# Kernel tuning notes

Hardware: AMD Instinct MI355X
Metric: run time of the kernel (lower is better)

## Reference

```python
import jax, jax.numpy as jnp
import numpy as np

B, F, H, E, C, K = 32768, 1024, 512, 10, 10, 4  # batch, in_features, hidden, f_enc, num_classes, n_branches


def setup_inputs() -> dict:
    key = jax.random.key(0)
    ks = jax.random.split(key, 12)
    def rn(k, shape, scale):
        return jax.random.normal(k, shape, jnp.float32) * scale
    return {
        "w0": rn(ks[0], (B, F), 1.0),
        "w1": rn(ks[1], (B, F), 1.0),
        "w2": rn(ks[2], (B, F), 1.0),
        "w3": rn(ks[3], (B, F), 1.0),
        # 4 branch linears in -> hidden, stacked on leading axis
        "Wlin": rn(ks[4], (K, H, F), F ** -0.5),
        "blin": jnp.zeros((K, H), jnp.float32),
        # per-branch Q/K/V projections hidden -> f_enc
        "Wq": rn(ks[5], (K, E, H), H ** -0.5),
        "bq": jnp.zeros((K, E), jnp.float32),
        "Wk": rn(ks[6], (K, E, H), H ** -0.5),
        "bk": jnp.zeros((K, E), jnp.float32),
        "Wv": rn(ks[7], (K, E, H), H ** -0.5),
        "bv": jnp.zeros((K, E), jnp.float32),
        # 4 final classifier heads f_enc -> num_classes
        "Wfin": rn(ks[8], (K, C, E), E ** -0.5),
        "bfin": jnp.zeros((K, C), jnp.float32),
    }


def reference(w0, w1, w2, w3, Wlin, blin, Wq, bq, Wk, bk, Wv, bv, Wfin, bfin):
    # dropout is identity in eval mode
    w = jnp.stack([w0, w1, w2, w3], axis=1)              # [B,K,F]
    h = jnp.einsum('bkf,khf->bkh', w, Wlin) + blin        # [B,K,H]
    q = jnp.einsum('bkh,keh->bke', h, Wq) + bq            # [B,K,E]
    k_enc = jnp.einsum('bkh,keh->bke', h, Wk) + bk        # [B,K,E]
    v = jnp.einsum('bkh,keh->bke', h, Wv) + bv            # [B,K,E]
    # einsum 'bij,bil->bjl' contracts the branch axis (i == K)
    attn = jnp.einsum('bke,bkl->bel', q, k_enc) / np.float32(np.sqrt(E))  # [B,E,E]
    attn = jax.nn.softmax(attn, axis=1)                   # torch Softmax(dim=1)
    att_out = jnp.einsum('bnm,bkm->bkn', attn, v)         # [B,K,E]
    w0o = att_out[:, 0, :]                                # original uses index 0 for all four heads
    logits = jnp.einsum('be,kce->bkc', w0o, Wfin) + bfin  # [B,K,C]
    outputs = jnp.mean(jax.nn.softmax(logits, axis=-1), axis=1)  # 0.25 * sum of 4 softmaxed heads
    return (outputs, attn)
```

## Files before the change

kernel.cpp:

```cpp
#include <hip/hip_runtime.h>
#include <stdint.h>

#define B_ROWS 32768
#define F_DIM  1024
#define H_DIM  512

typedef __attribute__((ext_vector_type(4))) float    floatx4;
typedef __attribute__((ext_vector_type(2))) __fp16   fp16x2;
typedef __attribute__((ext_vector_type(8))) _Float16 halfx8;

__device__ __forceinline__ void async_load16(const void* g, void* l) {
    __builtin_amdgcn_global_load_lds(
        (const __attribute__((address_space(1))) void*)g,
        (__attribute__((address_space(3))) void*)l, 16, 0, 0);
}

__device__ __forceinline__ floatx4 nt_load4(const float* p) {
    return __builtin_nontemporal_load((const floatx4*)p);
}

__global__ __launch_bounds__(128) void k_prep(
    const float* __restrict__ Wlin, const float* __restrict__ blin,
    const float* __restrict__ Wq, const float* __restrict__ Wk,
    const float* __restrict__ Wv, const float* __restrict__ bq,
    const float* __restrict__ bk, const float* __restrict__ bv,
    ushort* __restrict__ Wcomb16, float* __restrict__ bcomb)
{
    __shared__ float sw_[H_DIM];
    __shared__ float sbl[H_DIM];
    const int bx   = blockIdx.x;
    const int k    = bx >> 6;
    const int d    = (bx >> 1) & 31;
    const int half = bx & 1;
    const int t    = threadIdx.x;
    const int col  = half * 512 + t * 4;
    ushort4* outp = (ushort4*)(Wcomb16 + (((size_t)(k * 32 + d)) << 10) + col);

    if (d >= 30) {
        ushort4 z; z.x = z.y = z.z = z.w = 0;
        *outp = z;
        if (half == 0 && t == 0) bcomb[k * 32 + d] = 0.f;
        return;
    }

    const float* wrow; float bias;
    if (d < 10)      { wrow = Wq + (size_t)(k * 10 + d) * H_DIM;      bias = bq[k * 10 + d]; }
    else if (d < 20) { wrow = Wk + (size_t)(k * 10 + d - 10) * H_DIM; bias = bk[k * 10 + d - 10]; }
    else             { wrow = Wv + (size_t)(k * 10 + d - 20) * H_DIM; bias = bv[k * 10 + d - 20]; }

    const float* bl = blin + (size_t)k * H_DIM;
    for (int i = t; i < H_DIM; i += 128) { sw_[i] = wrow[i]; sbl[i] = bl[i]; }
    __syncthreads();

    const float* wl = Wlin + (((size_t)k * H_DIM) << 10) + col;

    floatx4 acc0 = {0.f,0.f,0.f,0.f}, acc1 = {0.f,0.f,0.f,0.f};
    float ba0 = 0.f, ba1 = 0.f;
    #pragma unroll 8
    for (int h = 0; h < H_DIM; h += 2) {
        const float s0 = sw_[h], s1 = sw_[h + 1];
        const floatx4 x0 = *(const floatx4*)(wl + ((size_t)h << 10));
        const floatx4 x1 = *(const floatx4*)(wl + ((size_t)(h + 1) << 10));
        acc0 += x0 * s0;
        acc1 += x1 * s1;
        ba0 += s0 * sbl[h];
        ba1 += s1 * sbl[h + 1];
    }
    const floatx4 acc = acc0 + acc1;
    union { _Float16 h[4]; ushort4 u; } o;
    o.h[0] = (_Float16)acc.x; o.h[1] = (_Float16)acc.y;
    o.h[2] = (_Float16)acc.z; o.h[3] = (_Float16)acc.w;
    *outp = o.u;
    if (half == 0 && t == 0) bcomb[k * 32 + d] = bias + ba0 + ba1;
}

#define SM_BS    0
#define SM_QKV   (64 * 1024)
#define SM_BC    (SM_QKV + 128 * 121 * 4)
#define SM_W     (SM_BC + 512)
#define SM_B     (SM_W + 1600)
#define SM_TOTAL (SM_B + 160)

__global__ __launch_bounds__(512) void k_all(
    const float* __restrict__ w0, const float* __restrict__ w1,
    const float* __restrict__ w2, const float* __restrict__ w3,
    const ushort* __restrict__ Wcomb16, const float* __restrict__ bcomb,
    const float* __restrict__ Wfin, const float* __restrict__ bfin,
    float* __restrict__ outputs, float* __restrict__ attn)
{
    __shared__ __align__(16) unsigned char smem[SM_TOTAL];
    ushort* Bs  = (ushort*)(smem + SM_BS);
    float*  QKV = (float*) (smem + SM_QKV);
    float*  sbc = (float*) (smem + SM_BC);
    float*  sW  = (float*) (smem + SM_W);
    float*  sb  = (float*) (smem + SM_B);
    float*  sA  = (float*) (smem + SM_BS);

    const int tid     = threadIdx.x;
    const int rowBase = blockIdx.x * 128;

    if (tid < 128) sbc[tid] = bcomb[tid];
    if (tid < 400) sW[tid]  = Wfin[tid];
    if (tid < 40)  sb[tid]  = bfin[tid];

    const int wv = tid >> 6;
    const int ln = tid & 63;
    const int lr = ln & 15;
    const int lq = ln >> 4;
    const int sw = lr & 7;

    #pragma unroll 1
    for (int k = 0; k < 4; ++k) {
        const float* A = (k == 0) ? w0 : (k == 1) ? w1 : (k == 2) ? w2 : w3;

        __syncthreads();
        #pragma unroll
        for (int it = 0; it < 8; ++it) {
            const int s   = it * 512 + tid;
            const int row = s >> 7;
            const int g   = (s & 127) ^ (row & 7);
            async_load16(Wcomb16 + (((size_t)(k * 32 + row)) << 10) + g * 8,
                         (ushort*)Bs + (size_t)s * 8);
        }
        __syncthreads();

        const float* aP = A + (size_t)(rowBase + wv * 16 + lr) * F_DIM + lq * 8;

        floatx4 acc0 = {0.f,0.f,0.f,0.f};
        floatx4 acc1 = {0.f,0.f,0.f,0.f};

#define COMPUTE(t, b0, b1) do {                                              \
    union { fp16x2 h2[4]; halfx8 h8; } u;                                    \
    u.h2[0] = __builtin_amdgcn_cvt_pkrtz(b0.x, b0.y);                        \
    u.h2[1] = __builtin_amdgcn_cvt_pkrtz(b0.z, b0.w);                        \
    u.h2[2] = __builtin_amdgcn_cvt_pkrtz(b1.x, b1.y);                        \
    u.h2[3] = __builtin_amdgcn_cvt_pkrtz(b1.z, b1.w);                        \
    const int slot_ = (((t) * 4 + lq) ^ sw) * 8;                             \
    const halfx8 bf0 = *(const halfx8*)&Bs[(lr << 10) + slot_];              \
    const halfx8 bf1 = *(const halfx8*)&Bs[((16 + lr) << 10) + slot_];       \
    acc0 = __builtin_amdgcn_mfma_f32_16x16x32_f16(u.h8, bf0, acc0, 0, 0, 0); \
    acc1 = __builtin_amdgcn_mfma_f32_16x16x32_f16(u.h8, bf1, acc1, 0, 0, 0); \
} while (0)

        floatx4 a0, a1, c0, c1;
        a0 = nt_load4(aP);
        a1 = nt_load4(aP + 4);
        #pragma unroll 4
        for (int t = 0; t < 32; t += 2) {
            c0 = nt_load4(aP + (t + 1) * 32);
            c1 = nt_load4(aP + (t + 1) * 32 + 4);
            COMPUTE(t, a0, a1);
            if (t + 2 < 32) {
                a0 = nt_load4(aP + (t + 2) * 32);
                a1 = nt_load4(aP + (t + 2) * 32 + 4);
            }
            COMPUTE(t + 1, c0, c1);
        }
#undef COMPUTE

        const int r0 = wv * 16 + lq * 4;
        #pragma unroll
        for (int r = 0; r < 4; ++r)
            QKV[(r0 + r) * 121 + k * 30 + lr] = acc0[r] + sbc[k * 32 + lr];
        const int d1 = 16 + lr;
        if (d1 < ((k == 0) ? 30 : 20)) {
            #pragma unroll
            for (int r = 0; r < 4; ++r)
                QKV[(r0 + r) * 121 + k * 30 + d1] = acc1[r] + sbc[k * 32 + d1];
        }
    }
    __syncthreads();

    float oc[10];
    if (tid < 128) {
        const float* Q = &QKV[tid * 121];
        float q[4][10], kk[4][10], v0[10];
        #pragma unroll
        for (int k = 0; k < 4; ++k)
            #pragma unroll
            for (int e = 0; e < 10; ++e) {
                q[k][e]  = Q[k * 30 + e];
                kk[k][e] = Q[k * 30 + 10 + e];
            }
        #pragma unroll
        for (int m = 0; m < 10; ++m) v0[m] = Q[20 + m];

        float out0[10];
        #pragma unroll
        for (int e = 0; e < 10; ++e) out0[e] = 0.f;
        float* sAr = &sA[tid * 101];
        const float inv = 0.31622776601683794f;

        #pragma unroll
        for (int m = 0; m < 10; ++m) {
            float col[10]; float mx = -1e30f;
            #pragma unroll
            for (int e = 0; e < 10; ++e) {
                col[e] = (q[0][e]*kk[0][m] + q[1][e]*kk[1][m]
                        + q[2][e]*kk[2][m] + q[3][e]*kk[3][m]) * inv;
                mx = fmaxf(mx, col[e]);
            }
            float s = 0.f;
            #pragma unroll
            for (int e = 0; e < 10; ++e) { col[e] = __expf(col[e] - mx); s += col[e]; }
            const float r = 1.f / s;
            #pragma unroll
            for (int e = 0; e < 10; ++e) {
                const float a = col[e] * r;
                sAr[e * 10 + m] = a;
                out0[e] += a * v0[m];
            }
        }

        #pragma unroll
        for (int c = 0; c < 10; ++c) oc[c] = 0.f;
        #pragma unroll
        for (int k = 0; k < 4; ++k) {
            float lg[10]; float mx = -1e30f;
            #pragma unroll
            for (int c = 0; c < 10; ++c) {
                float s = sb[k * 10 + c];
                #pragma unroll
                for (int e = 0; e < 10; ++e) s += out0[e] * sW[(k * 10 + c) * 10 + e];
                lg[c] = s; mx = fmaxf(mx, s);
            }
            float s = 0.f;
            #pragma unroll
            for (int c = 0; c < 10; ++c) { lg[c] = __expf(lg[c] - mx); s += lg[c]; }
            const float r = 0.25f / s;
            #pragma unroll
            for (int c = 0; c < 10; ++c) oc[c] += lg[c] * r;
        }
    }

    __syncthreads();
    const size_t abase = (size_t)blockIdx.x * 12800;
    for (int i = tid; i < 12800; i += 512) {
        const int bl = i / 100;
        attn[abase + i] = sA[bl * 101 + (i - bl * 100)];
    }

    __syncthreads();
    if (tid < 128) {
        #pragma unroll
        for (int c = 0; c < 10; ++c) sA[tid * 11 + c] = oc[c];
    }
    __syncthreads();
    const size_t obase = (size_t)blockIdx.x * 1280;
    for (int i = tid; i < 1280; i += 512) {
        const int bl = i / 10;
        outputs[obase + i] = sA[bl * 11 + (i - bl * 10)];
    }
}

extern "C" void kernel_launch(void* const* d_in, const int* in_sizes, int n_in,
                              void* d_out, int out_size, void* d_ws, size_t ws_size,
                              hipStream_t stream) {
    const float* w0   = (const float*)d_in[0];
    const float* w1   = (const float*)d_in[1];
    const float* w2   = (const float*)d_in[2];
    const float* w3   = (const float*)d_in[3];
    const float* Wlin = (const float*)d_in[4];
    const float* blin = (const float*)d_in[5];
    const float* Wq   = (const float*)d_in[6];
    const float* bq   = (const float*)d_in[7];
    const float* Wk   = (const float*)d_in[8];
    const float* bk   = (const float*)d_in[9];
    const float* Wv   = (const float*)d_in[10];
    const float* bv   = (const float*)d_in[11];
    const float* Wfin = (const float*)d_in[12];
    const float* bfin = (const float*)d_in[13];

    char* ws = (char*)d_ws;
    ushort* Wcomb16 = (ushort*)ws;
    float*  bcomb   = (float*)(ws + ((size_t)256 << 10));

    float* outputs = (float*)d_out;
    float* attn    = outputs + (size_t)B_ROWS * 10;

    k_prep<<<256, 128, 0, stream>>>(Wlin, blin, Wq, Wk, Wv, bq, bk, bv, Wcomb16, bcomb);
    k_all <<<256, 512, 0, stream>>>(w0, w1, w2, w3, Wcomb16, bcomb, Wfin, bfin, outputs, attn);
}
```

Before: 547.5 us.

## Software-pipeline A loads and next-branch weight prefetch across fully unrolled loop

Fully unrolls the four-branch by 32-step GEMM loop into one 128-step stream. It keeps an 8-deep register ring of activation loads that runs across branch boundaries, and prefetches the next branch's fp16 weight tile into registers during the current branch, storing it to LDS between barriers. The aim is to remove the pipeline drain and exposed latency at each branch switch. It also requests two blocks per CU via launch bounds. The cost is much higher register pressure (16 float4 plus 8 uint4 buffers), which under the occupancy hint could cause spills.

```diff
diff --git a/kernel.cpp b/kernel.cpp
--- a/kernel.cpp
+++ b/kernel.cpp
@@ -81,7 +81,7 @@
 #define SM_B     (SM_W + 1600)
 #define SM_TOTAL (SM_B + 160)
 
-__global__ __launch_bounds__(512) void k_all(
+__global__ __launch_bounds__(512, 2) void k_all(
     const float* __restrict__ w0, const float* __restrict__ w1,
     const float* __restrict__ w2, const float* __restrict__ w3,
     const ushort* __restrict__ Wcomb16, const float* __restrict__ bcomb,
@@ -109,64 +109,91 @@
     const int lq = ln >> 4;
     const int sw = lr & 7;
 
-    #pragma unroll 1
-    for (int k = 0; k < 4; ++k) {
-        const float* A = (k == 0) ? w0 : (k == 1) ? w1 : (k == 2) ? w2 : w3;
-
-        __syncthreads();
-        #pragma unroll
-        for (int it = 0; it < 8; ++it) {
-            const int s   = it * 512 + tid;
-            const int row = s >> 7;
-            const int g   = (s & 127) ^ (row & 7);
-            async_load16(Wcomb16 + (((size_t)(k * 32 + row)) << 10) + g * 8,
-                         (ushort*)Bs + (size_t)s * 8);
-        }
-        __syncthreads();
-
-        const float* aP = A + (size_t)(rowBase + wv * 16 + lr) * F_DIM + lq * 8;
-
-        floatx4 acc0 = {0.f,0.f,0.f,0.f};
-        floatx4 acc1 = {0.f,0.f,0.f,0.f};
-
-#define COMPUTE(t, b0, b1) do {                                              \
-    union { fp16x2 h2[4]; halfx8 h8; } u;                                    \
-    u.h2[0] = __builtin_amdgcn_cvt_pkrtz(b0.x, b0.y);                        \
-    u.h2[1] = __builtin_amdgcn_cvt_pkrtz(b0.z, b0.w);                        \
-    u.h2[2] = __builtin_amdgcn_cvt_pkrtz(b1.x, b1.y);                        \
-    u.h2[3] = __builtin_amdgcn_cvt_pkrtz(b1.z, b1.w);                        \
-    const int slot_ = (((t) * 4 + lq) ^ sw) * 8;                             \
-    const halfx8 bf0 = *(const halfx8*)&Bs[(lr << 10) + slot_];              \
-    const halfx8 bf1 = *(const halfx8*)&Bs[((16 + lr) << 10) + slot_];       \
-    acc0 = __builtin_amdgcn_mfma_f32_16x16x32_f16(u.h8, bf0, acc0, 0, 0, 0); \
-    acc1 = __builtin_amdgcn_mfma_f32_16x16x32_f16(u.h8, bf1, acc1, 0, 0, 0); \
-} while (0)
-
-        floatx4 a0, a1, c0, c1;
-        a0 = nt_load4(aP);
-        a1 = nt_load4(aP + 4);
-        #pragma unroll 4
-        for (int t = 0; t < 32; t += 2) {
-            c0 = nt_load4(aP + (t + 1) * 32);
-            c1 = nt_load4(aP + (t + 1) * 32 + 4);
-            COMPUTE(t, a0, a1);
-            if (t + 2 < 32) {
-                a0 = nt_load4(aP + (t + 2) * 32);
-                a1 = nt_load4(aP + (t + 2) * 32 + 4);
-            }
-            COMPUTE(t + 1, c0, c1);
-        }
-#undef COMPUTE
-
-        const int r0 = wv * 16 + lq * 4;
-        #pragma unroll
-        for (int r = 0; r < 4; ++r)
-            QKV[(r0 + r) * 121 + k * 30 + lr] = acc0[r] + sbc[k * 32 + lr];
-        const int d1 = 16 + lr;
-        if (d1 < ((k == 0) ? 30 : 20)) {
+    #pragma unroll
+    for (int it = 0; it < 8; ++it) {
+        const int s   = it * 512 + tid;
+        const int row = s >> 7;
+        const int g   = (s & 127) ^ (row & 7);
+        async_load16(Wcomb16 + (((size_t)row) << 10) + g * 8,
+                     (ushort*)Bs + (size_t)s * 8);
+    }
+    __syncthreads();
+
+    const size_t aoff = (size_t)(rowBase + wv * 16 + lr) * F_DIM + lq * 8;
+    const float* aPk[4] = { w0 + aoff, w1 + aoff, w2 + aoff, w3 + aoff };
+
+    floatx4 abuf[16];
+    #pragma unroll
+    for (int s = 0; s < 8; ++s) {
+        abuf[(s & 7) * 2]     = nt_load4(aPk[0] + s * 32);
+        abuf[(s & 7) * 2 + 1] = nt_load4(aPk[0] + s * 32 + 4);
+    }
+
+    uint4 breg[8];
+    floatx4 acc0 = {0.f,0.f,0.f,0.f};
+    floatx4 acc1 = {0.f,0.f,0.f,0.f};
+
+    #pragma unroll
+    for (int s = 0; s < 128; ++s) {
+        const int k = s >> 5;
+        const int t = s & 31;
+
+        if (t == 0 && s > 0) {
+            __builtin_amdgcn_s_barrier();
+            #pragma unroll
+            for (int it = 0; it < 8; ++it)
+                *(uint4*)((ushort*)Bs + (size_t)(it * 512 + tid) * 8) = breg[it];
+            asm volatile("s_waitcnt lgkmcnt(0)" ::: "memory");
+            __builtin_amdgcn_sched_barrier(0);
+            __builtin_amdgcn_s_barrier();
+            acc0 = (floatx4){0.f,0.f,0.f,0.f};
+            acc1 = (floatx4){0.f,0.f,0.f,0.f};
+        }
+
+        if (t == 1 && k < 3) {
+            #pragma unroll
+            for (int it = 0; it < 8; ++it) {
+                const int sl  = it * 512 + tid;
+                const int row = sl >> 7;
+                const int g   = (sl & 127) ^ (row & 7);
+                breg[it] = *(const uint4*)(Wcomb16 +
+                              (((size_t)((k + 1) * 32 + row)) << 10) + g * 8);
+            }
+        }
+
+        {
+            const floatx4 b0 = abuf[(s & 7) * 2];
+            const floatx4 b1 = abuf[(s & 7) * 2 + 1];
+            union { fp16x2 h2[4]; halfx8 h8; } u;
+            u.h2[0] = __builtin_amdgcn_cvt_pkrtz(b0.x, b0.y);
+            u.h2[1] = __builtin_amdgcn_cvt_pkrtz(b0.z, b0.w);
+            u.h2[2] = __builtin_amdgcn_cvt_pkrtz(b1.x, b1.y);
+            u.h2[3] = __builtin_amdgcn_cvt_pkrtz(b1.z, b1.w);
+            const int slot_ = ((t * 4 + lq) ^ sw) * 8;
+            const halfx8 bf0 = *(const halfx8*)&Bs[(lr << 10) + slot_];
+            const halfx8 bf1 = *(const halfx8*)&Bs[((16 + lr) << 10) + slot_];
+            acc0 = __builtin_amdgcn_mfma_f32_16x16x32_f16(u.h8, bf0, acc0, 0, 0, 0);
+            acc1 = __builtin_amdgcn_mfma_f32_16x16x32_f16(u.h8, bf1, acc1, 0, 0, 0);
+        }
+
+        if (s + 8 < 128) {
+            const int kn = (s + 8) >> 5;
+            const int tn = (s + 8) & 31;
+            abuf[(s & 7) * 2]     = nt_load4(aPk[kn] + tn * 32);
+            abuf[(s & 7) * 2 + 1] = nt_load4(aPk[kn] + tn * 32 + 4);
+        }
+
+        if (t == 31) {
+            const int r0 = wv * 16 + lq * 4;
             #pragma unroll
             for (int r = 0; r < 4; ++r)
-                QKV[(r0 + r) * 121 + k * 30 + d1] = acc1[r] + sbc[k * 32 + d1];
+                QKV[(r0 + r) * 121 + k * 30 + lr] = acc0[r] + sbc[k * 32 + lr];
+            const int d1 = 16 + lr;
+            if (d1 < ((k == 0) ? 30 : 20)) {
+                #pragma unroll
+                for (int r = 0; r < 4; ++r)
+                    QKV[(r0 + r) * 121 + k * 30 + d1] = acc1[r] + sbc[k * 32 + d1];
+            }
         }
     }
     __syncthreads();
```

Measured after the change: 719.4 us. +31.4%, slower.
